# Kernel optimization log

Measured on AMD Instinct MI355X. Metric: run time of the kernel, lower is better.

## Reference

```python
import jax, jax.numpy as jnp
import numpy as np

N_TOK = 384          # sentence length n
SEQ = N_TOK + 2      # + START, STOP
H = 256              # lstm_dim (per-direction hidden)
EMB = 128            # tag_embedding_dim == word_embedding_dim (embeddings are summed)
TAGV, WORDV, LABV = 64, 10000, 128
LABH = SPLH = 256


def _lstm_dir(x, Wx, Wh, b, reverse=False):
    # x: [S, EMB]; Wx: [4H, EMB]; Wh: [4H, H]; b: [4H]. PyTorch gate order i,f,g,o.
    Hdim = Wh.shape[1]

    def cell(carry, xt):
        h, c = carry
        g = Wx @ xt + Wh @ h + b
        i, f, gg, o = jnp.split(g, 4)
        c = jax.nn.sigmoid(f) * c + jax.nn.sigmoid(i) * jnp.tanh(gg)
        h = jax.nn.sigmoid(o) * jnp.tanh(c)
        return (h, c), h

    init = (jnp.zeros((Hdim,), x.dtype), jnp.zeros((Hdim,), x.dtype))
    _, hs = jax.lax.scan(cell, init, x, reverse=reverse)
    return hs  # [S, H]


def _mlp(x, w1, b1, w2, b2):
    return jnp.maximum(x @ w1.T + b1, 0.0) @ w2.T + b2


def setup_inputs() -> dict:
    key = jax.random.key(0)
    ks = jax.random.split(key, 18)
    s = 0.05
    return {
        'tag_ids': jax.random.randint(ks[0], (SEQ,), 0, TAGV, dtype=jnp.int32),
        'word_ids': jax.random.randint(ks[1], (SEQ,), 0, WORDV, dtype=jnp.int32),
        'tag_emb': jax.random.normal(ks[2], (TAGV, EMB), jnp.float32) * s,
        'word_emb': jax.random.normal(ks[3], (WORDV, EMB), jnp.float32) * s,
        'wxf': jax.random.normal(ks[4], (4 * H, EMB), jnp.float32) * s,
        'whf': jax.random.normal(ks[5], (4 * H, H), jnp.float32) * s,
        'bf': jax.random.normal(ks[6], (4 * H,), jnp.float32) * s,
        'wxb': jax.random.normal(ks[7], (4 * H, EMB), jnp.float32) * s,
        'whb': jax.random.normal(ks[8], (4 * H, H), jnp.float32) * s,
        'bb': jax.random.normal(ks[9], (4 * H,), jnp.float32) * s,
        'lab_w1': jax.random.normal(ks[10], (LABH, 2 * H), jnp.float32) * s,
        'lab_b1': jax.random.normal(ks[11], (LABH,), jnp.float32) * s,
        'lab_w2': jax.random.normal(ks[12], (LABV, LABH), jnp.float32) * s,
        'lab_b2': jax.random.normal(ks[13], (LABV,), jnp.float32) * s,
        'spl_w1': jax.random.normal(ks[14], (SPLH, 2 * H), jnp.float32) * s,
        'spl_b1': jax.random.normal(ks[15], (SPLH,), jnp.float32) * s,
        'spl_w2': jax.random.normal(ks[16], (1, SPLH), jnp.float32) * s,
        'spl_b2': jax.random.normal(ks[17], (1,), jnp.float32) * s,
    }


def reference(tag_ids, word_ids, tag_emb, word_emb, wxf, whf, bf, wxb, whb, bb,
              lab_w1, lab_b1, lab_w2, lab_b2, spl_w1, spl_b1, spl_w2, spl_b2):
    n = tag_ids.shape[0] - 2
    # token embeddings: tag + word (as in parse())
    emb = tag_emb[tag_ids] + word_emb[word_ids]            # [S, EMB]
    hf = _lstm_dir(emb, wxf, whf, bf, reverse=False)        # [S, H] forward dir
    hb = _lstm_dir(emb, wxb, whb, bb, reverse=True)         # [S, H] backward dir
    # span encoding for every (left, right), 0 <= left,right <= n:
    #   fwd = hf[right] - hf[left];  bwd = hb[left+1] - hb[right+1]
    f = hf[: n + 1]                                         # [n+1, H]
    b1 = hb[1 : n + 2]                                      # [n+1, H]
    enc_f = f[None, :, :] - f[:, None, :]                   # [l, r, H]
    enc_b = b1[:, None, :] - b1[None, :, :]                 # [l, r, H]
    enc = jnp.concatenate([enc_f, enc_b], axis=-1)          # [n+1, n+1, 2H]
    # batched f_label / f_split over the whole chart
    label_scores = _mlp(enc, lab_w1, lab_b1, lab_w2, lab_b2)  # [n+1, n+1, LABV]
    split_scores = _mlp(enc, spl_w1, spl_b1, spl_w2, spl_b2)  # [n+1, n+1, 1]
    return jnp.concatenate([label_scores, split_scores], axis=-1)  # [n+1, n+1, LABV+1]
```

## Files before the change

kernel.cpp:

```cpp
#include <hip/hip_runtime.h>
#include <cstdint>

#define SEQ   386
#define NP1   385
#define HDIM  256
#define G4    1024
#define EMBD  128
#define LABV  128
#define OUTC  129

typedef _Float16 h2 __attribute__((ext_vector_type(2)));
typedef _Float16 f16x8 __attribute__((ext_vector_type(8)));
typedef float    f32x4 __attribute__((ext_vector_type(4)));

__device__ __forceinline__ uint32_t pack2(float a, float b) {
    h2 v; v[0] = (_Float16)a; v[1] = (_Float16)b;
    return __builtin_bit_cast(uint32_t, v);
}

__device__ __forceinline__ float dot2(uint32_t wa, uint32_t hb, float c) {
    h2 a = __builtin_bit_cast(h2, wa);
    h2 b = __builtin_bit_cast(h2, hb);
#if __has_builtin(__builtin_amdgcn_fdot2)
    return __builtin_amdgcn_fdot2(a, b, c, false);
#else
    return fmaf((float)a[1], (float)b[1], fmaf((float)a[0], (float)b[0], c));
#endif
}

__device__ __forceinline__ float sigm(float x) { return 1.f / (1.f + __expf(-x)); }
__device__ __forceinline__ float ftanh(float x) {
    x = fminf(fmaxf(x, -15.f), 15.f);
    float e = __expf(2.f * x);
    return (e - 1.f) / (e + 1.f);
}

#define OFF_EMB   0u
#define OFF_GX    197632u
#define OFF_WREG  3359744u
#define OFF_WLDS  4146176u
#define OFF_F     4408320u
#define OFF_B     4802560u
#define OFF_DL    5196800u
#define OFF_DS    5591040u
#define OFF_W2F   5985280u

__global__ void k_embed(const int* __restrict__ tag_ids, const int* __restrict__ word_ids,
                        const float* __restrict__ tag_emb, const float* __restrict__ word_emb,
                        float* __restrict__ emb) {
    int t = blockIdx.x, d = threadIdx.x;
    emb[t * EMBD + d] = tag_emb[tag_ids[t] * EMBD + d] + word_emb[word_ids[t] * EMBD + d];
}

__global__ __launch_bounds__(256) void k_gx(const float* __restrict__ emb,
                                            const float* __restrict__ wxf, const float* __restrict__ bf_,
                                            const float* __restrict__ wxb, const float* __restrict__ bb_,
                                            float* __restrict__ gx) {
    const int dir = blockIdx.y;
    const int t0  = blockIdx.x * 8;
    const float* Wx   = dir ? wxb : wxf;
    const float* bias = dir ? bb_ : bf_;
    __shared__ float se[8 * EMBD];
    for (int idx = threadIdx.x; idx < 8 * EMBD; idx += 256) {
        int tt = t0 + (idx >> 7);
        se[idx] = (tt < SEQ) ? emb[tt * EMBD + (idx & 127)] : 0.f;
    }
    __syncthreads();
    const float4* se4 = (const float4*)se;
    for (int q = 0; q < 4; ++q) {
        int r = threadIdx.x + q * 256;
        float bv = bias[r];
        float acc[8];
#pragma unroll
        for (int tt = 0; tt < 8; ++tt) acc[tt] = bv;
        const float4* wrow = (const float4*)(Wx + r * EMBD);
        for (int d4 = 0; d4 < 32; ++d4) {
            float4 w = wrow[d4];
#pragma unroll
            for (int tt = 0; tt < 8; ++tt) {
                float4 e = se4[tt * 32 + d4];
                acc[tt] += w.x * e.x + w.y * e.y + w.z * e.z + w.w * e.w;
            }
        }
        for (int tt = 0; tt < 8; ++tt) {
            int t = t0 + tt;
            if (t < SEQ) gx[(dir * SEQ + t) * G4 + r] = acc[tt];
        }
    }
}

__global__ void k_wconv(const float* __restrict__ whf, const float* __restrict__ whb,
                        uint4* __restrict__ wreg, uint32_t* __restrict__ wlds) {
    const int dir = blockIdx.x;
    const float* Wh = dir ? whb : whf;
    const int y = blockIdx.y, tid = threadIdx.x;
    if (y < 96) {
        int idx = y * 256 + tid;
        int r = idx / 24, cg = idx % 24;
        const float* src = Wh + r * HDIM + cg * 8;
        uint4 o;
        o.x = pack2(src[0], src[1]); o.y = pack2(src[2], src[3]);
        o.z = pack2(src[4], src[5]); o.w = pack2(src[6], src[7]);
        wreg[dir * 24576 + cg * 1024 + r] = o;
    } else {
        int idx = (y - 96) * 256 + tid;
        int r = idx >> 5, c = idx & 31;
        wlds[dir * 32768 + r * 32 + c] = pack2(Wh[r * HDIM + 192 + 2 * c], Wh[r * HDIM + 193 + 2 * c]);
    }
}

__global__ __launch_bounds__(512)
__attribute__((amdgpu_waves_per_eu(2, 2)))
void k_lstm(const uint4* __restrict__ wreg,
            const uint32_t* __restrict__ wlds,
            const float* __restrict__ gx,
            float* __restrict__ fout, float* __restrict__ bout) {
    const int dir = blockIdx.x;
    const int tid = threadIdx.x;
    __shared__ uint32_t wl[1024 * 36];
    __shared__ float gbuf[1024];
    __shared__ __align__(16) uint32_t hsh[136];

    const uint32_t* wsrc = wlds + dir * 32768;
    for (int idx = tid; idx < 32768; idx += 512)
        wl[(idx >> 5) * 36 + (idx & 31)] = wsrc[idx];
    if (tid < 136) hsh[tid] = 0u;

    uint4 w0[24], w1[24];
    const uint4* wr = wreg + dir * 24576;
#pragma unroll
    for (int g = 0; g < 24; ++g) {
        w0[g] = wr[g * 1024 + tid];
        w1[g] = wr[g * 1024 + tid + 512];
    }

    const float* gxd = gx + dir * SEQ * G4;
    float c = 0.f;
    const int tfirst = dir ? (SEQ - 1) : 0;
    float gxv0 = gxd[tfirst * G4 + tid];
    float gxv1 = gxd[tfirst * G4 + tid + 512];
    __syncthreads();

    const uint4* h4 = (const uint4*)hsh;
    const uint4* wlr0 = (const uint4*)(wl + tid * 36);
    const uint4* wlr1 = (const uint4*)(wl + (tid + 512) * 36);

    for (int s = 0; s < SEQ; ++s) {
        int t = dir ? (SEQ - 1 - s) : s;
        float gn0 = 0.f, gn1 = 0.f;
        if (s < SEQ - 1) {
            int tn = dir ? (SEQ - 2 - s) : (s + 1);
            gn0 = gxd[tn * G4 + tid];
            gn1 = gxd[tn * G4 + tid + 512];
        }
        float a0 = gxv0, a1 = gxv1;
#pragma unroll
        for (int g = 0; g < 24; ++g) {
            uint4 hv = h4[g];
            a0 = dot2(w0[g].x, hv.x, a0);
            a0 = dot2(w0[g].y, hv.y, a0);
            a0 = dot2(w0[g].z, hv.z, a0);
            a0 = dot2(w0[g].w, hv.w, a0);
            a1 = dot2(w1[g].x, hv.x, a1);
            a1 = dot2(w1[g].y, hv.y, a1);
            a1 = dot2(w1[g].z, hv.z, a1);
            a1 = dot2(w1[g].w, hv.w, a1);
        }
#pragma unroll
        for (int g = 0; g < 8; ++g) {
            uint4 hv = h4[24 + g];
            uint4 v0 = wlr0[g];
            uint4 v1 = wlr1[g];
            a0 = dot2(v0.x, hv.x, a0);
            a0 = dot2(v0.y, hv.y, a0);
            a0 = dot2(v0.z, hv.z, a0);
            a0 = dot2(v0.w, hv.w, a0);
            a1 = dot2(v1.x, hv.x, a1);
            a1 = dot2(v1.y, hv.y, a1);
            a1 = dot2(v1.z, hv.z, a1);
            a1 = dot2(v1.w, hv.w, a1);
        }
        gbuf[tid] = a0;
        gbuf[tid + 512] = a1;
        __syncthreads();
        if (tid < HDIM) {
            float gi = gbuf[tid];
            float gf = gbuf[tid + 256];
            float gg = gbuf[tid + 512];
            float go = gbuf[tid + 768];
            c = sigm(gf) * c + sigm(gi) * ftanh(gg);
            float h = sigm(go) * ftanh(c);
            ((_Float16*)hsh)[tid] = (_Float16)h;
            if (!dir) { if (t < NP1) fout[t * HDIM + tid] = h; }
            else      { if (t >= 1)  bout[(t - 1) * HDIM + tid] = h; }
        }
        __syncthreads();
        gxv0 = gn0;
        gxv1 = gn1;
    }
}

__global__ __launch_bounds__(256) void k_dmat(const float* __restrict__ fm, const float* __restrict__ bm,
                                              const float* __restrict__ lw1, const float* __restrict__ sw1,
                                              float* __restrict__ dlab, float* __restrict__ dspl) {
    const int t0 = blockIdx.x * 8;
    const int tid = threadIdx.x;
    __shared__ float fs[8 * HDIM], bs[8 * HDIM];
    for (int idx = tid; idx < 8 * HDIM; idx += 256) {
        int tt = t0 + (idx >> 8);
        float fv = 0.f, bv = 0.f;
        if (tt < NP1) { fv = fm[tt * HDIM + (idx & 255)]; bv = bm[tt * HDIM + (idx & 255)]; }
        fs[idx] = fv; bs[idx] = bv;
    }
    __syncthreads();
    float al[8], asp[8];
#pragma unroll
    for (int q = 0; q < 8; ++q) { al[q] = 0.f; asp[q] = 0.f; }
    const float4* lrow = (const float4*)(lw1 + tid * 512);
    const float4* srow = (const float4*)(sw1 + tid * 512);
    const float4* fs4 = (const float4*)fs;
    const float4* bs4 = (const float4*)bs;
    for (int d4 = 0; d4 < 64; ++d4) {
        float4 wlv = lrow[d4], wsv = srow[d4];
#pragma unroll
        for (int tt = 0; tt < 8; ++tt) {
            float4 e = fs4[tt * 64 + d4];
            al[tt]  += wlv.x * e.x + wlv.y * e.y + wlv.z * e.z + wlv.w * e.w;
            asp[tt] += wsv.x * e.x + wsv.y * e.y + wsv.z * e.z + wsv.w * e.w;
        }
    }
    for (int d4 = 0; d4 < 64; ++d4) {
        float4 wlv = lrow[64 + d4], wsv = srow[64 + d4];
#pragma unroll
        for (int tt = 0; tt < 8; ++tt) {
            float4 e = bs4[tt * 64 + d4];
            al[tt]  -= wlv.x * e.x + wlv.y * e.y + wlv.z * e.z + wlv.w * e.w;
            asp[tt] -= wsv.x * e.x + wsv.y * e.y + wsv.z * e.z + wsv.w * e.w;
        }
    }
    for (int tt = 0; tt < 8; ++tt) {
        int t = t0 + tt;
        if (t < NP1) { dlab[t * HDIM + tid] = al[tt]; dspl[t * HDIM + tid] = asp[tt]; }
    }
}

__global__ void k_w2f(const float* __restrict__ lw2, _Float16* __restrict__ w2f) {
    int m = blockIdx.x, k = threadIdx.x;
    w2f[(((k >> 3) * LABV) + m) * 8 + (k & 7)] = (_Float16)lw2[m * HDIM + k];
}

__global__ __launch_bounds__(256) void k_out(const float* __restrict__ dlab, const float* __restrict__ dspl,
                                             const float* __restrict__ lb1, const float* __restrict__ sb1,
                                             const _Float16* __restrict__ w2f, const float* __restrict__ lb2,
                                             const float* __restrict__ sw2, const float* __restrict__ sb2,
                                             float* __restrict__ outp) {
    const int i = blockIdx.y, jtblk = blockIdx.x, tid = threadIdx.x;
    __shared__ float dli[HDIM], dsi[HDIM];
    __shared__ _Float16 hl[32 * 264];

    dli[tid] = dlab[i * HDIM + tid] - lb1[tid];
    dsi[tid] = dspl[i * HDIM + tid] - sb1[tid];
    __syncthreads();

    for (int j = 0; j < 32; ++j) {
        int jj = jtblk * 32 + j;
        float v = 0.f;
        if (jj < NP1) v = fmaxf(dlab[jj * HDIM + tid] - dli[tid], 0.f);
        hl[j * 264 + tid] = (_Float16)v;
    }

    {
        int w = tid >> 6, l = tid & 63;
        float sw2v[4];
#pragma unroll
        for (int cc = 0; cc < 4; ++cc) sw2v[cc] = sw2[l + 64 * cc];
        float sb2v = sb2[0];
        for (int q = 0; q < 8; ++q) {
            int jj = jtblk * 32 + w * 8 + q;
            if (jj < NP1) {
                float sum = 0.f;
#pragma unroll
                for (int cc = 0; cc < 4; ++cc) {
                    int k = l + 64 * cc;
                    float v = fmaxf(dspl[jj * HDIM + k] - dsi[k], 0.f);
                    sum += v * sw2v[cc];
                }
#pragma unroll
                for (int off = 32; off > 0; off >>= 1) sum += __shfl_down(sum, off, 64);
                if (l == 0) outp[(size_t)(i * NP1 + jj) * OUTC + 128] = sum + sb2v;
            }
        }
    }
    __syncthreads();

    const int w = tid >> 6, l = tid & 63;
    const int q = l >> 4, c16 = l & 15;
    f32x4 acc[2][2];
#pragma unroll
    for (int a = 0; a < 2; ++a)
#pragma unroll
        for (int b = 0; b < 2; ++b) acc[a][b] = (f32x4){0.f, 0.f, 0.f, 0.f};

    const int mt0 = w * 2;
#pragma unroll
    for (int kb = 0; kb < 8; ++kb) {
        f16x8 a0 = *(const f16x8*)(hl + (0 * 16 + c16) * 264 + kb * 32 + q * 8);
        f16x8 a1 = *(const f16x8*)(hl + (1 * 16 + c16) * 264 + kb * 32 + q * 8);
        f16x8 b0 = *(const f16x8*)(w2f + (((kb * 4 + q) * LABV) + mt0 * 16 + c16) * 8);
        f16x8 b1 = *(const f16x8*)(w2f + (((kb * 4 + q) * LABV) + (mt0 + 1) * 16 + c16) * 8);
        acc[0][0] = __builtin_amdgcn_mfma_f32_16x16x32_f16(a0, b0, acc[0][0], 0, 0, 0);
        acc[0][1] = __builtin_amdgcn_mfma_f32_16x16x32_f16(a0, b1, acc[0][1], 0, 0, 0);
        acc[1][0] = __builtin_amdgcn_mfma_f32_16x16x32_f16(a1, b0, acc[1][0], 0, 0, 0);
        acc[1][1] = __builtin_amdgcn_mfma_f32_16x16x32_f16(a1, b1, acc[1][1], 0, 0, 0);
    }

#pragma unroll
    for (int mb = 0; mb < 2; ++mb) {
        int m = (mt0 + mb) * 16 + c16;
        float bias = lb2[m];
#pragma unroll
        for (int jt = 0; jt < 2; ++jt) {
#pragma unroll
            for (int r = 0; r < 4; ++r) {
                int jj = jtblk * 32 + jt * 16 + q * 4 + r;
                if (jj < NP1) outp[(size_t)(i * NP1 + jj) * OUTC + m] = acc[jt][mb][r] + bias;
            }
        }
    }
}

extern "C" void kernel_launch(void* const* d_in, const int* in_sizes, int n_in,
                              void* d_out, int out_size, void* d_ws, size_t ws_size,
                              hipStream_t stream) {
    const int*   tag_ids  = (const int*)d_in[0];
    const int*   word_ids = (const int*)d_in[1];
    const float* tag_emb  = (const float*)d_in[2];
    const float* word_emb = (const float*)d_in[3];
    const float* wxf = (const float*)d_in[4];
    const float* whf = (const float*)d_in[5];
    const float* bf_ = (const float*)d_in[6];
    const float* wxb = (const float*)d_in[7];
    const float* whb = (const float*)d_in[8];
    const float* bb_ = (const float*)d_in[9];
    const float* lw1 = (const float*)d_in[10];
    const float* lb1 = (const float*)d_in[11];
    const float* lw2 = (const float*)d_in[12];
    const float* lb2 = (const float*)d_in[13];
    const float* sw1 = (const float*)d_in[14];
    const float* sb1 = (const float*)d_in[15];
    const float* sw2 = (const float*)d_in[16];
    const float* sb2 = (const float*)d_in[17];

    char* ws = (char*)d_ws;
    float*     emb  = (float*)(ws + OFF_EMB);
    float*     gx   = (float*)(ws + OFF_GX);
    uint4*     wreg = (uint4*)(ws + OFF_WREG);
    uint32_t*  wlds = (uint32_t*)(ws + OFF_WLDS);
    float*     fm   = (float*)(ws + OFF_F);
    float*     bm   = (float*)(ws + OFF_B);
    float*     dlab = (float*)(ws + OFF_DL);
    float*     dspl = (float*)(ws + OFF_DS);
    _Float16*  w2f  = (_Float16*)(ws + OFF_W2F);
    float*     outp = (float*)d_out;

    k_embed<<<dim3(SEQ), dim3(EMBD), 0, stream>>>(tag_ids, word_ids, tag_emb, word_emb, emb);
    k_gx   <<<dim3(49, 2), dim3(256), 0, stream>>>(emb, wxf, bf_, wxb, bb_, gx);
    k_wconv<<<dim3(2, 224), dim3(256), 0, stream>>>(whf, whb, wreg, wlds);
    k_w2f  <<<dim3(LABV), dim3(HDIM), 0, stream>>>(lw2, w2f);
    k_lstm <<<dim3(2), dim3(512), 0, stream>>>(wreg, wlds, gx, fm, bm);
    k_dmat <<<dim3(49), dim3(256), 0, stream>>>(fm, bm, lw1, sw1, dlab, dspl);
    k_out  <<<dim3(13, NP1), dim3(256), 0, stream>>>(dlab, dspl, lb1, sb1, w2f, lb2, sw2, sb2, outp);
}
```

Before: 890.0 us.

## Split each LSTM direction across four workgroups with global-memory flag sync

Each LSTM direction's gate rows are partitioned across four workgroups, so every thread holds its fp16 Wh slice in 16 registers instead of splitting weights between registers and LDS. Workgroups swap their slice of h through double-buffered global slots each step, guarded by release/acquire step counters. The grid is 26 blocks with only those where bid&7 < 2 active, apparently so that blocks of one direction share a cache domain. This trades per-step matvec work for a cross-workgroup spin-wait each step. The counters are never reset and the spin has a bounded break, so stale values from a previous call could let waits pass early and produce a race.

```diff
diff --git a/kernel.cpp b/kernel.cpp
--- a/kernel.cpp
+++ b/kernel.cpp
@@ -37,13 +37,13 @@
 
 #define OFF_EMB   0u
 #define OFF_GX    197632u
-#define OFF_WREG  3359744u
-#define OFF_WLDS  4146176u
+#define OFF_WR2   3359744u
 #define OFF_F     4408320u
 #define OFF_B     4802560u
 #define OFF_DL    5196800u
 #define OFF_DS    5591040u
 #define OFF_W2F   5985280u
+#define OFF_SYNC  6050816u
 
 __global__ void k_embed(const int* __restrict__ tag_ids, const int* __restrict__ word_ids,
                         const float* __restrict__ tag_emb, const float* __restrict__ word_emb,
@@ -89,114 +89,128 @@
     }
 }
 
-__global__ void k_wconv(const float* __restrict__ whf, const float* __restrict__ whb,
-                        uint4* __restrict__ wreg, uint32_t* __restrict__ wlds) {
-    const int dir = blockIdx.x;
-    const float* Wh = dir ? whb : whf;
-    const int y = blockIdx.y, tid = threadIdx.x;
-    if (y < 96) {
-        int idx = y * 256 + tid;
-        int r = idx / 24, cg = idx % 24;
-        const float* src = Wh + r * HDIM + cg * 8;
+__global__ void k_wconv2(const float* __restrict__ whf, const float* __restrict__ whb,
+                         uint4* __restrict__ wreg2) {
+    const int d = blockIdx.x;
+    const float* Wh = d ? whb : whf;
+    int idx = blockIdx.y * 256 + threadIdx.x;
+    int q = idx >> 9, t = idx & 511;
+    int ch = t >> 8, lr = t & 255, g = lr >> 6, ul = lr & 63;
+    int r = g * 256 + q * 64 + ul;
+    const float* src = Wh + r * HDIM + ch * 128;
+    uint4* dst = wreg2 + ((size_t)(d * 4 + q) * 512 + t) * 16;
+    for (int i = 0; i < 16; ++i) {
+        const float* s8 = src + i * 8;
         uint4 o;
-        o.x = pack2(src[0], src[1]); o.y = pack2(src[2], src[3]);
-        o.z = pack2(src[4], src[5]); o.w = pack2(src[6], src[7]);
-        wreg[dir * 24576 + cg * 1024 + r] = o;
-    } else {
-        int idx = (y - 96) * 256 + tid;
-        int r = idx >> 5, c = idx & 31;
-        wlds[dir * 32768 + r * 32 + c] = pack2(Wh[r * HDIM + 192 + 2 * c], Wh[r * HDIM + 193 + 2 * c]);
-    }
-}
-
-__global__ __launch_bounds__(512)
-__attribute__((amdgpu_waves_per_eu(2, 2)))
-void k_lstm(const uint4* __restrict__ wreg,
-            const uint32_t* __restrict__ wlds,
-            const float* __restrict__ gx,
-            float* __restrict__ fout, float* __restrict__ bout) {
-    const int dir = blockIdx.x;
+        o.x = pack2(s8[0], s8[1]); o.y = pack2(s8[2], s8[3]);
+        o.z = pack2(s8[4], s8[5]); o.w = pack2(s8[6], s8[7]);
+        dst[i] = o;
+    }
+}
+
+__global__ __launch_bounds__(512) void k_lstm(const uint4* __restrict__ wreg2,
+                                              const float* __restrict__ gx,
+                                              float* __restrict__ fout, float* __restrict__ bout,
+                                              uint32_t* __restrict__ sync) {
+    const int bid = blockIdx.x;
+    const int d = bid & 7, q = bid >> 3;
+    if (d >= 2) return;
+
     const int tid = threadIdx.x;
-    __shared__ uint32_t wl[1024 * 36];
-    __shared__ float gbuf[1024];
-    __shared__ __align__(16) uint32_t hsh[136];
-
-    const uint32_t* wsrc = wlds + dir * 32768;
-    for (int idx = tid; idx < 32768; idx += 512)
-        wl[(idx >> 5) * 36 + (idx & 31)] = wsrc[idx];
-    if (tid < 136) hsh[tid] = 0u;
-
-    uint4 w0[24], w1[24];
-    const uint4* wr = wreg + dir * 24576;
-#pragma unroll
-    for (int g = 0; g < 24; ++g) {
-        w0[g] = wr[g * 1024 + tid];
-        w1[g] = wr[g * 1024 + tid + 512];
-    }
-
-    const float* gxd = gx + dir * SEQ * G4;
+    const int ch = tid >> 8;
+    const int lr = tid & 255;
+    const int g = lr >> 6, ul = lr & 63;
+    const int grow = g * 256 + q * 64 + ul;
+
+    __shared__ float gbuf[512];
+    __shared__ float ggate[256];
+    __shared__ __align__(16) _Float16 hsh[256];
+
+    uint4 w[16];
+    {
+        const uint4* wp = wreg2 + ((size_t)(d * 4 + q) * 512 + tid) * 16;
+#pragma unroll
+        for (int i = 0; i < 16; ++i) w[i] = wp[i];
+    }
+
+    if (tid < 128) ((uint32_t*)hsh)[tid] = 0u;
+
+    const float* gxd = gx + d * SEQ * G4;
+    const int tfirst = d ? (SEQ - 1) : 0;
     float c = 0.f;
-    const int tfirst = dir ? (SEQ - 1) : 0;
-    float gxv0 = gxd[tfirst * G4 + tid];
-    float gxv1 = gxd[tfirst * G4 + tid + 512];
-    __syncthreads();
-
-    const uint4* h4 = (const uint4*)hsh;
-    const uint4* wlr0 = (const uint4*)(wl + tid * 36);
-    const uint4* wlr1 = (const uint4*)(wl + (tid + 512) * 36);
+    float gxv = (tid < 256) ? gxd[tfirst * G4 + grow] : 0.f;
+
+    uint32_t* slot = sync + (d * 4 + q) * 128;
+    __syncthreads();
+
+    const uint4* hp = ((const uint4*)hsh) + ch * 16;
 
     for (int s = 0; s < SEQ; ++s) {
-        int t = dir ? (SEQ - 1 - s) : s;
-        float gn0 = 0.f, gn1 = 0.f;
-        if (s < SEQ - 1) {
-            int tn = dir ? (SEQ - 2 - s) : (s + 1);
-            gn0 = gxd[tn * G4 + tid];
-            gn1 = gxd[tn * G4 + tid + 512];
-        }
-        float a0 = gxv0, a1 = gxv1;
-#pragma unroll
-        for (int g = 0; g < 24; ++g) {
-            uint4 hv = h4[g];
-            a0 = dot2(w0[g].x, hv.x, a0);
-            a0 = dot2(w0[g].y, hv.y, a0);
-            a0 = dot2(w0[g].z, hv.z, a0);
-            a0 = dot2(w0[g].w, hv.w, a0);
-            a1 = dot2(w1[g].x, hv.x, a1);
-            a1 = dot2(w1[g].y, hv.y, a1);
-            a1 = dot2(w1[g].z, hv.z, a1);
-            a1 = dot2(w1[g].w, hv.w, a1);
-        }
-#pragma unroll
-        for (int g = 0; g < 8; ++g) {
-            uint4 hv = h4[24 + g];
-            uint4 v0 = wlr0[g];
-            uint4 v1 = wlr1[g];
-            a0 = dot2(v0.x, hv.x, a0);
-            a0 = dot2(v0.y, hv.y, a0);
-            a0 = dot2(v0.z, hv.z, a0);
-            a0 = dot2(v0.w, hv.w, a0);
-            a1 = dot2(v1.x, hv.x, a1);
-            a1 = dot2(v1.y, hv.y, a1);
-            a1 = dot2(v1.z, hv.z, a1);
-            a1 = dot2(v1.w, hv.w, a1);
-        }
-        gbuf[tid] = a0;
-        gbuf[tid + 512] = a1;
+        int t = d ? (SEQ - 1 - s) : s;
+
+        float acc = 0.f;
+#pragma unroll
+        for (int i = 0; i < 16; ++i) {
+            uint4 hv = hp[i];
+            acc = dot2(w[i].x, hv.x, acc);
+            acc = dot2(w[i].y, hv.y, acc);
+            acc = dot2(w[i].z, hv.z, acc);
+            acc = dot2(w[i].w, hv.w, acc);
+        }
+        gbuf[tid] = acc;
         __syncthreads();
-        if (tid < HDIM) {
-            float gi = gbuf[tid];
-            float gf = gbuf[tid + 256];
-            float gg = gbuf[tid + 512];
-            float go = gbuf[tid + 768];
+
+        float gn = 0.f;
+        if (tid < 256) {
+            if (s < SEQ - 1) {
+                int tn = d ? (SEQ - 2 - s) : (s + 1);
+                gn = gxd[tn * G4 + grow];
+            }
+            ggate[lr] = gbuf[tid] + gbuf[tid + 256] + gxv;
+        }
+        __syncthreads();
+
+        if (tid < 64) {
+            float gi = ggate[tid];
+            float gf = ggate[64 + tid];
+            float gg = ggate[128 + tid];
+            float go = ggate[192 + tid];
             c = sigm(gf) * c + sigm(gi) * ftanh(gg);
             float h = sigm(go) * ftanh(c);
-            ((_Float16*)hsh)[tid] = (_Float16)h;
-            if (!dir) { if (t < NP1) fout[t * HDIM + tid] = h; }
-            else      { if (t >= 1)  bout[(t - 1) * HDIM + tid] = h; }
+            int ug = q * 64 + tid;
+            hsh[ug] = (_Float16)h;
+            if (!d) { if (t < NP1) fout[t * HDIM + ug] = h; }
+            else    { if (t >= 1)  bout[(t - 1) * HDIM + ug] = h; }
+        }
+        if (tid < 32) {
+            uint32_t payv = *((const uint32_t*)&hsh[q * 64 + tid * 2]);
+            __hip_atomic_store(slot + (s & 1) * 32 + tid, payv,
+                               __ATOMIC_RELAXED, __HIP_MEMORY_SCOPE_AGENT);
+        }
+        if (tid == 0) {
+            __hip_atomic_store(slot + 64, (uint32_t)(s + 1),
+                               __ATOMIC_RELEASE, __HIP_MEMORY_SCOPE_AGENT);
+        }
+        if (tid >= 448 && tid < 451) {
+            int j = tid - 448;
+            int pq = j + (j >= q);
+            const uint32_t* pc = sync + (d * 4 + pq) * 128 + 64;
+            int guard = 0;
+            while ((int)__hip_atomic_load(pc, __ATOMIC_ACQUIRE, __HIP_MEMORY_SCOPE_AGENT)
+                   < (int)(s + 1)) {
+                if (++guard > (1 << 16)) break;
+            }
         }
         __syncthreads();
-        gxv0 = gn0;
-        gxv1 = gn1;
+        if (tid < 96) {
+            int j = tid >> 5, lane = tid & 31;
+            int pq = j + (j >= q);
+            uint32_t v = __hip_atomic_load(sync + (d * 4 + pq) * 128 + (s & 1) * 32 + lane,
+                                           __ATOMIC_RELAXED, __HIP_MEMORY_SCOPE_AGENT);
+            *((uint32_t*)&hsh[pq * 64 + lane * 2]) = v;
+        }
+        gxv = gn;
+        __syncthreads();
     }
 }
 
@@ -352,22 +366,22 @@
     const float* sb2 = (const float*)d_in[17];
 
     char* ws = (char*)d_ws;
-    float*     emb  = (float*)(ws + OFF_EMB);
-    float*     gx   = (float*)(ws + OFF_GX);
-    uint4*     wreg = (uint4*)(ws + OFF_WREG);
-    uint32_t*  wlds = (uint32_t*)(ws + OFF_WLDS);
-    float*     fm   = (float*)(ws + OFF_F);
-    float*     bm   = (float*)(ws + OFF_B);
-    float*     dlab = (float*)(ws + OFF_DL);
-    float*     dspl = (float*)(ws + OFF_DS);
-    _Float16*  w2f  = (_Float16*)(ws + OFF_W2F);
-    float*     outp = (float*)d_out;
-
-    k_embed<<<dim3(SEQ), dim3(EMBD), 0, stream>>>(tag_ids, word_ids, tag_emb, word_emb, emb);
-    k_gx   <<<dim3(49, 2), dim3(256), 0, stream>>>(emb, wxf, bf_, wxb, bb_, gx);
-    k_wconv<<<dim3(2, 224), dim3(256), 0, stream>>>(whf, whb, wreg, wlds);
-    k_w2f  <<<dim3(LABV), dim3(HDIM), 0, stream>>>(lw2, w2f);
-    k_lstm <<<dim3(2), dim3(512), 0, stream>>>(wreg, wlds, gx, fm, bm);
-    k_dmat <<<dim3(49), dim3(256), 0, stream>>>(fm, bm, lw1, sw1, dlab, dspl);
-    k_out  <<<dim3(13, NP1), dim3(256), 0, stream>>>(dlab, dspl, lb1, sb1, w2f, lb2, sw2, sb2, outp);
-}
+    float*     emb   = (float*)(ws + OFF_EMB);
+    float*     gx    = (float*)(ws + OFF_GX);
+    uint4*     wreg2 = (uint4*)(ws + OFF_WR2);
+    float*     fm    = (float*)(ws + OFF_F);
+    float*     bm    = (float*)(ws + OFF_B);
+    float*     dlab  = (float*)(ws + OFF_DL);
+    float*     dspl  = (float*)(ws + OFF_DS);
+    _Float16*  w2f   = (_Float16*)(ws + OFF_W2F);
+    uint32_t*  syncp = (uint32_t*)(ws + OFF_SYNC);
+    float*     outp  = (float*)d_out;
+
+    k_embed <<<dim3(SEQ), dim3(EMBD), 0, stream>>>(tag_ids, word_ids, tag_emb, word_emb, emb);
+    k_gx    <<<dim3(49, 2), dim3(256), 0, stream>>>(emb, wxf, bf_, wxb, bb_, gx);
+    k_wconv2<<<dim3(2, 8), dim3(256), 0, stream>>>(whf, whb, wreg2);
+    k_w2f   <<<dim3(LABV), dim3(HDIM), 0, stream>>>(lw2, w2f);
+    k_lstm  <<<dim3(26), dim3(512), 0, stream>>>(wreg2, gx, fm, bm, syncp);
+    k_dmat  <<<dim3(49), dim3(256), 0, stream>>>(fm, bm, lw1, sw1, dlab, dspl);
+    k_out   <<<dim3(13, NP1), dim3(256), 0, stream>>>(dlab, dspl, lb1, sb1, w2f, lb2, sw2, sb2, outp);
+}
```

Result: slower. 1.212 ms (+36.2%).
